# Kernel optimization log

Hardware: AMD Instinct MI355X
Metric: run time of the kernel (lower is better)

The kernel has to match this reference:

```python
import jax, jax.numpy as jnp
import numpy as np

HIDDEN = 2048
N_HEAD = 16
N_KV_HEAD = 4
HEAD_DIM = HIDDEN // N_HEAD
B, S = 2, 2048


def setup_inputs() -> dict:
    key = jax.random.key(0)
    ks = jax.random.split(key, 10)
    scale = 1.0 / np.sqrt(HIDDEN)
    x = jax.random.normal(ks[0], (B, S, HIDDEN), dtype=jnp.float32)
    # causal additive mask, broadcastable over batch and heads
    causal = jnp.tril(jnp.ones((S, S), dtype=jnp.bool_))
    attention_mask = jnp.where(causal, 0.0, -1e9).astype(jnp.float32)[None, None]
    wq_w = jax.random.uniform(ks[1], (HIDDEN, HIDDEN), jnp.float32, -scale, scale)
    wq_b = jax.random.uniform(ks[2], (HIDDEN,), jnp.float32, -scale, scale)
    wk_w = jax.random.uniform(ks[3], (N_KV_HEAD * HEAD_DIM, HIDDEN), jnp.float32, -scale, scale)
    wk_b = jax.random.uniform(ks[4], (N_KV_HEAD * HEAD_DIM,), jnp.float32, -scale, scale)
    wv_w = jax.random.uniform(ks[5], (N_KV_HEAD * HEAD_DIM, HIDDEN), jnp.float32, -scale, scale)
    wv_b = jax.random.uniform(ks[6], (N_KV_HEAD * HEAD_DIM,), jnp.float32, -scale, scale)
    wo_w = jax.random.uniform(ks[7], (HIDDEN, HIDDEN), jnp.float32, -scale, scale)
    wo_b = jax.random.uniform(ks[8], (HIDDEN,), jnp.float32, -scale, scale)
    return dict(x=x, attention_mask=attention_mask, wq_w=wq_w, wq_b=wq_b,
                wk_w=wk_w, wk_b=wk_b, wv_w=wv_w, wv_b=wv_b, wo_w=wo_w, wo_b=wo_b)


def reference(x, attention_mask, wq_w, wq_b, wk_w, wk_b, wv_w, wv_b, wo_w, wo_b):
    bs, seq_len, _ = x.shape
    group = N_HEAD // N_KV_HEAD
    q = x @ wq_w.T + wq_b  # [B,S,H*D]
    k = x @ wk_w.T + wk_b  # [B,S,Hkv*D]
    v = x @ wv_w.T + wv_b
    q = q.reshape(bs, seq_len, N_HEAD, HEAD_DIM).transpose(0, 2, 1, 3)        # [B,H,S,D]
    k = k.reshape(bs, seq_len, N_KV_HEAD, HEAD_DIM).transpose(0, 2, 1, 3)     # [B,Hkv,S,D]
    v = v.reshape(bs, seq_len, N_KV_HEAD, HEAD_DIM).transpose(0, 2, 1, 3)
    # GQA: share each kv head across `group` query heads (repeat_interleave equiv)
    qg = q.reshape(bs, N_KV_HEAD, group, seq_len, HEAD_DIM)
    scores = jnp.einsum('bkgqd,bkld->bkgql', qg, k) / np.sqrt(HEAD_DIM)       # [B,Hkv,g,S,S]
    scores = scores + attention_mask[:, :, None]  # mask broadcast over head dims
    attn = jax.nn.softmax(scores, axis=-1)  # dropout is identity at inference
    out = jnp.einsum('bkgql,bkld->bkgqd', attn, v)                             # [B,Hkv,g,S,D]
    out = out.reshape(bs, N_HEAD, seq_len, HEAD_DIM).transpose(0, 2, 1, 3)
    out = out.reshape(bs, seq_len, HIDDEN)
    return out @ wo_w.T + wo_b
```

## Files before the change

kernel.cpp:

```cpp
#include <hip/hip_runtime.h>

typedef __bf16 bf16;
typedef __bf16 bf16x8 __attribute__((ext_vector_type(8)));
typedef __bf16 bf16x4 __attribute__((ext_vector_type(4)));
typedef __bf16 bf16x2 __attribute__((ext_vector_type(2)));
typedef float  f32x4  __attribute__((ext_vector_type(4)));

#define HIDDEN 2048
#define NH 16
#define NKV 4
#define HD 128
#define BB 2
#define SS 2048
#define MTOT (BB*SS)
#define KVD (NKV*HD)

__device__ __forceinline__ void gload_lds16(const void* g, void* l) {
  __builtin_amdgcn_global_load_lds(
      (__attribute__((address_space(1))) void*)(void*)g,
      (__attribute__((address_space(3))) void*)l,
      16, 0, 0);
}

__device__ __forceinline__ void pipe_barrier() {
  __builtin_amdgcn_sched_barrier(0);
  __builtin_amdgcn_s_barrier();
  __builtin_amdgcn_sched_barrier(0);
}

__global__ void detect_dtype(const unsigned short* __restrict__ x, int* __restrict__ flag) {
  __shared__ int cnt;
  if (threadIdx.x == 0) cnt = 0;
  __syncthreads();
  int c = 0;
  for (int i = threadIdx.x; i < 8192; i += blockDim.x) {
    float v = fabsf(__uint_as_float((unsigned)x[i] << 16));
    if (v > 64.0f || (v > 0.0f && v < 9.5367431640625e-07f)) ++c;
  }
  atomicAdd(&cnt, c);
  __syncthreads();
  if (threadIdx.x == 0) flag[0] = (cnt > 1024) ? 1 : 0;
}

struct ConvJobs {
  const void* src[8];
  bf16*       dst[8];
  long long   n[8];
};

__global__ void conv_multi(ConvJobs jobs, const int* __restrict__ flag) {
  const int f = flag[0];
  const int a = blockIdx.y;
  const long long n = jobs.n[a];
  bf16* dst = jobs.dst[a];
  long long i = (long long)blockIdx.x * blockDim.x + threadIdx.x;
  const long long stride = (long long)gridDim.x * blockDim.x;
  if (f) {
    const float* s = (const float*)jobs.src[a];
    for (; i < n; i += stride) dst[i] = (bf16)s[i];
  } else {
    const bf16* s = (const bf16*)jobs.src[a];
    for (; i < n; i += stride) dst[i] = s[i];
  }
}

__global__ void conv_one(const void* __restrict__ src, bf16* __restrict__ dst,
                         long long n, const int* __restrict__ flag) {
  const int f = flag[0];
  long long i = (long long)blockIdx.x * blockDim.x + threadIdx.x;
  const long long stride = (long long)gridDim.x * blockDim.x;
  if (f) {
    const float* s = (const float*)src;
    for (; i < n; i += stride) dst[i] = (bf16)s[i];
  } else {
    const bf16* s = (const bf16*)src;
    for (; i < n; i += stride) dst[i] = s[i];
  }
}


__global__ __launch_bounds__(512)
void gemm_qkv256(const bf16* __restrict__ A,
                 const bf16* __restrict__ wq, const bf16* __restrict__ bq,
                 const bf16* __restrict__ wk, const bf16* __restrict__ bk,
                 const bf16* __restrict__ wv, const bf16* __restrict__ bv,
                 bf16* __restrict__ Cq, bf16* __restrict__ Ck, bf16* __restrict__ Cvt)
{
  __shared__ bf16 Asl[2][256*32];
  __shared__ bf16 Bsl[2][256*32];
  const int bx = blockIdx.x;
  const bf16 *Wp, *bias;
  int n0, mode;
  if (bx < 8)       { Wp = wq; bias = bq; n0 = bx*256;      mode = 0; }
  else if (bx < 10) { Wp = wk; bias = bk; n0 = (bx-8)*256;  mode = 1; }
  else              { Wp = wv; bias = bv; n0 = (bx-10)*256; mode = 2; }

  const int tid  = threadIdx.x;
  const int wave = tid >> 6, lane = tid & 63;
  const int g = lane >> 4, l15 = lane & 15;
  const int wr = wave >> 2, wc = wave & 3;
  const int m0 = blockIdx.y * 256;

  f32x4 acc[8][4] = {};

  auto stage4 = [&](int nb, int k0) {
    #pragma unroll
    for (int i = 0; i < 2; ++i) {
      const int cl  = tid + i*512;
      const int row = cl >> 2, ch = cl & 3;
      const int sc  = ch ^ ((row >> 2) & 3);
      gload_lds16(A  + (size_t)(m0 + row)*HIDDEN + k0 + sc*8, &Asl[nb][cl*8]);
      gload_lds16(Wp + (size_t)(n0 + row)*HIDDEN + k0 + sc*8, &Bsl[nb][cl*8]);
    }
  };

  stage4(0, 0);
  asm volatile("s_waitcnt vmcnt(0)" ::: "memory");
  pipe_barrier();

  const int nt = HIDDEN / 32;
  int buf = 0;
  for (int t = 0; t < nt; ++t) {
    bf16x8 af[4], bfr[4];
    #pragma unroll
    for (int mi = 0; mi < 4; ++mi) {
      const int rl = wr*128 + mi*16 + l15;
      const int ch = g ^ ((rl >> 2) & 3);
      af[mi] = *(const bf16x8*)&Asl[buf][rl*32 + ch*8];
    }
    #pragma unroll
    for (int ni = 0; ni < 4; ++ni) {
      const int rl = wc*64 + ni*16 + l15;
      const int ch = g ^ ((rl >> 2) & 3);
      bfr[ni] = *(const bf16x8*)&Bsl[buf][rl*32 + ch*8];
    }
    if (t + 1 < nt) stage4(buf ^ 1, (t + 1) * 32);
    pipe_barrier();
    __builtin_amdgcn_s_setprio(1);
    #pragma unroll
    for (int mi = 0; mi < 4; ++mi)
      #pragma unroll
      for (int ni = 0; ni < 4; ++ni)
        acc[mi][ni] = __builtin_amdgcn_mfma_f32_16x16x32_bf16(af[mi], bfr[ni], acc[mi][ni], 0, 0, 0);
    __builtin_amdgcn_s_setprio(0);
    #pragma unroll
    for (int mi = 0; mi < 4; ++mi) {
      const int rl = wr*128 + 64 + mi*16 + l15;
      const int ch = g ^ ((rl >> 2) & 3);
      af[mi] = *(const bf16x8*)&Asl[buf][rl*32 + ch*8];
    }
    pipe_barrier();
    __builtin_amdgcn_s_setprio(1);
    #pragma unroll
    for (int mi = 0; mi < 4; ++mi)
      #pragma unroll
      for (int ni = 0; ni < 4; ++ni)
        acc[4+mi][ni] = __builtin_amdgcn_mfma_f32_16x16x32_bf16(af[mi], bfr[ni], acc[4+mi][ni], 0, 0, 0);
    __builtin_amdgcn_s_setprio(0);
    __builtin_amdgcn_sched_barrier(0);
    asm volatile("s_waitcnt vmcnt(0)" ::: "memory");
    __builtin_amdgcn_s_barrier();
    __builtin_amdgcn_sched_barrier(0);
    buf ^= 1;
  }

  if (mode == 2) {
    #pragma unroll
    for (int ni = 0; ni < 4; ++ni) {
      const int cc = n0 + wc*64 + ni*16 + l15;
      const float bv2 = (float)bias[cc];
      #pragma unroll
      for (int mi = 0; mi < 8; ++mi) {
        const int row = m0 + wr*128 + mi*16 + g*4;
        bf16x4 o4;
        #pragma unroll
        for (int r = 0; r < 4; ++r) o4[r] = (bf16)(acc[mi][ni][r] + bv2);
        *(bf16x4*)&Cvt[(size_t)cc*MTOT + row] = o4;
      }
    }
  } else {
    bf16* Cb = (mode == 0) ? Cq : Ck;
    const int N = (mode == 0) ? HIDDEN : KVD;
    #pragma unroll
    for (int ni = 0; ni < 4; ++ni) {
      const int col = n0 + wc*64 + ni*16 + l15;
      const float bv2 = (float)bias[col];
      #pragma unroll
      for (int mi = 0; mi < 8; ++mi) {
        const int row = m0 + wr*128 + mi*16 + g*4;
        #pragma unroll
        for (int r = 0; r < 4; ++r)
          Cb[(size_t)(row + r)*N + col] = (bf16)(acc[mi][ni][r] + bv2);
      }
    }
  }
}

__global__ __launch_bounds__(512)
void gemm_o256(const bf16* __restrict__ A, const bf16* __restrict__ Wp,
               const bf16* __restrict__ bias, void* __restrict__ C,
               int N, int K, const int* __restrict__ flagp)
{
  __shared__ bf16 Asl[2][256*32];
  __shared__ bf16 Bsl[2][256*32];
  const int tid  = threadIdx.x;
  const int wave = tid >> 6, lane = tid & 63;
  const int g = lane >> 4, l15 = lane & 15;
  const int wr = wave >> 2, wc = wave & 3;
  const int m0 = blockIdx.y * 256, n0 = blockIdx.x * 256;

  f32x4 acc[8][4] = {};

  auto stage4 = [&](int nb, int k0) {
    #pragma unroll
    for (int i = 0; i < 2; ++i) {
      const int cl  = tid + i*512;
      const int row = cl >> 2, ch = cl & 3;
      const int sc  = ch ^ ((row >> 2) & 3);
      gload_lds16(A  + (size_t)(m0 + row)*K + k0 + sc*8, &Asl[nb][cl*8]);
      gload_lds16(Wp + (size_t)(n0 + row)*K + k0 + sc*8, &Bsl[nb][cl*8]);
    }
  };

  stage4(0, 0);
  asm volatile("s_waitcnt vmcnt(0)" ::: "memory");
  pipe_barrier();

  const int nt = K / 32;
  int buf = 0;
  for (int t = 0; t < nt; ++t) {
    bf16x8 af[4], bfr[4];
    #pragma unroll
    for (int mi = 0; mi < 4; ++mi) {
      const int rl = wr*128 + mi*16 + l15;
      const int ch = g ^ ((rl >> 2) & 3);
      af[mi] = *(const bf16x8*)&Asl[buf][rl*32 + ch*8];
    }
    #pragma unroll
    for (int ni = 0; ni < 4; ++ni) {
      const int rl = wc*64 + ni*16 + l15;
      const int ch = g ^ ((rl >> 2) & 3);
      bfr[ni] = *(const bf16x8*)&Bsl[buf][rl*32 + ch*8];
    }
    if (t + 1 < nt) stage4(buf ^ 1, (t + 1) * 32);
    pipe_barrier();
    __builtin_amdgcn_s_setprio(1);
    #pragma unroll
    for (int mi = 0; mi < 4; ++mi)
      #pragma unroll
      for (int ni = 0; ni < 4; ++ni)
        acc[mi][ni] = __builtin_amdgcn_mfma_f32_16x16x32_bf16(af[mi], bfr[ni], acc[mi][ni], 0, 0, 0);
    __builtin_amdgcn_s_setprio(0);
    #pragma unroll
    for (int mi = 0; mi < 4; ++mi) {
      const int rl = wr*128 + 64 + mi*16 + l15;
      const int ch = g ^ ((rl >> 2) & 3);
      af[mi] = *(const bf16x8*)&Asl[buf][rl*32 + ch*8];
    }
    pipe_barrier();
    __builtin_amdgcn_s_setprio(1);
    #pragma unroll
    for (int mi = 0; mi < 4; ++mi)
      #pragma unroll
      for (int ni = 0; ni < 4; ++ni)
        acc[4+mi][ni] = __builtin_amdgcn_mfma_f32_16x16x32_bf16(af[mi], bfr[ni], acc[4+mi][ni], 0, 0, 0);
    __builtin_amdgcn_s_setprio(0);
    __builtin_amdgcn_sched_barrier(0);
    asm volatile("s_waitcnt vmcnt(0)" ::: "memory");
    __builtin_amdgcn_s_barrier();
    __builtin_amdgcn_sched_barrier(0);
    buf ^= 1;
  }

  const int outf = flagp ? flagp[0] : 0;
  if (outf) {
    float* Cf = (float*)C;
    #pragma unroll
    for (int ni = 0; ni < 4; ++ni) {
      const int col = n0 + wc*64 + ni*16 + l15;
      const float bv = (float)bias[col];
      #pragma unroll
      for (int mi = 0; mi < 8; ++mi) {
        const int row = m0 + wr*128 + mi*16 + g*4;
        #pragma unroll
        for (int r = 0; r < 4; ++r)
          Cf[(size_t)(row + r)*N + col] = acc[mi][ni][r] + bv;
      }
    }
  } else {
    bf16* Cb = (bf16*)C;
    #pragma unroll
    for (int ni = 0; ni < 4; ++ni) {
      const int col = n0 + wc*64 + ni*16 + l15;
      const float bv = (float)bias[col];
      #pragma unroll
      for (int mi = 0; mi < 8; ++mi) {
        const int row = m0 + wr*128 + mi*16 + g*4;
        #pragma unroll
        for (int r = 0; r < 4; ++r)
          Cb[(size_t)(row + r)*N + col] = (bf16)(acc[mi][ni][r] + bv);
      }
    }
  }
}

#define QB 64
#define PPAD 72

__global__ __launch_bounds__(256)
void attn_fwd(const bf16* __restrict__ Q, const bf16* __restrict__ K,
              const bf16* __restrict__ Vt, bf16* __restrict__ O)
{
  __shared__ bf16 Ks[2][64*128];
  __shared__ bf16 Vs[2][128*64];
  __shared__ bf16 Pl[4][16][PPAD];
  const int tid = threadIdx.x, wave = tid >> 6, lane = tid & 63;
  const int g = lane >> 4, l15 = lane & 15;
  const int bh = blockIdx.y;
  const int b = bh >> 4, h = bh & 15, kvh = h >> 2;
  const bf16* Qh = Q + ((size_t)b*SS)*HIDDEN + h*HD;
  const bf16* Kh = K + ((size_t)b*SS)*KVD + kvh*HD;
  const bf16* Vh = Vt + ((size_t)kvh*HD)*MTOT + (size_t)b*SS;
  bf16*       Oh = O + ((size_t)b*SS)*HIDDEN + h*HD;

  const float scale  = 0.08838834764831845f;
  const float L2E    = 1.4426950408889634f;
  const float NEGBIG = -1.0e30f;

  const int krow_st = (lane >> 4);
  const int vrow_st = (lane >> 3);
  const int ksc     = (lane & 15);
  const int vsc     = (lane & 7) ^ (lane >> 3);

  #pragma unroll 1
  for (int pass = 0; pass < 2; ++pass) {
    const int qt = pass ? (31 - (int)blockIdx.x) : (int)blockIdx.x;
    const int qrow0 = qt*QB + wave*16;
    const int qg    = qrow0 + l15;

    bf16x8 bq[4];
    #pragma unroll
    for (int c = 0; c < 4; ++c)
      bq[c] = *(const bf16x8*)(Qh + (size_t)(qrow0 + l15)*HIDDEN + c*32 + g*8);

    f32x4 od[8] = {};
    float m_run = NEGBIG, l_part = 0.f;
    const int ntiles = qt + 1;

    {
      const int kv0 = 0;
      #pragma unroll
      for (int i = 0; i < 4; ++i) {
        const int s = wave*4 + i;
        const int kr = s*4 + krow_st;
        const int kc = ksc ^ (kr & 7);
        gload_lds16(Kh + (size_t)(kv0 + kr)*KVD + kc*8, &Ks[0][s*512 + lane*8]);
        const int vr = s*8 + vrow_st;
        gload_lds16(Vh + (size_t)vr*MTOT + kv0 + vsc*8, &Vs[0][s*512 + lane*8]);
      }
    }
    asm volatile("s_waitcnt vmcnt(0)" ::: "memory");
    __syncthreads();

    int buf = 0;
    #pragma unroll 1
    for (int t = 0; t < ntiles; ++t) {
      const int kv0 = t * 64;

      if (t + 1 < ntiles) {
        const int kv1 = kv0 + 64;
        #pragma unroll
        for (int i = 0; i < 4; ++i) {
          const int s = wave*4 + i;
          const int kr = s*4 + krow_st;
          const int kc = ksc ^ (kr & 7);
          gload_lds16(Kh + (size_t)(kv1 + kr)*KVD + kc*8, &Ks[buf^1][s*512 + lane*8]);
          const int vr = s*8 + vrow_st;
          gload_lds16(Vh + (size_t)vr*MTOT + kv1 + vsc*8, &Vs[buf^1][s*512 + lane*8]);
        }
      }

      f32x4 st[4];
      #pragma unroll
      for (int nb = 0; nb < 4; ++nb) {
        f32x4 s = {};
        #pragma unroll
        for (int c = 0; c < 4; ++c) {
          const int krow = nb*16 + l15;
          const int kch  = (c*4 + g) ^ (krow & 7);
          bf16x8 ka = *(const bf16x8*)&Ks[buf][krow*128 + kch*8];
          s = __builtin_amdgcn_mfma_f32_16x16x32_bf16(ka, bq[c], s, 0, 0, 0);
        }
        st[nb] = s;
      }

      float x[16];
      float mt = NEGBIG;
      #pragma unroll
      for (int nb = 0; nb < 4; ++nb)
        #pragma unroll
        for (int r = 0; r < 4; ++r) {
          const int kv = kv0 + nb*16 + g*4 + r;
          float v = st[nb][r] * scale;
          v = (kv <= qg) ? v : NEGBIG;
          x[nb*4 + r] = v;
          mt = fmaxf(mt, v);
        }
      mt = fmaxf(mt, __shfl_xor(mt, 16, 64));
      mt = fmaxf(mt, __shfl_xor(mt, 32, 64));
      const float m_new = fmaxf(m_run, mt);
      const float corr  = __builtin_amdgcn_exp2f((m_run - m_new) * L2E);

      float psum = 0.f;
      bf16x2 pk[4][2];
      #pragma unroll
      for (int nb = 0; nb < 4; ++nb) {
        const float p0 = __builtin_amdgcn_exp2f((x[nb*4+0] - m_new) * L2E);
        const float p1 = __builtin_amdgcn_exp2f((x[nb*4+1] - m_new) * L2E);
        const float p2 = __builtin_amdgcn_exp2f((x[nb*4+2] - m_new) * L2E);
        const float p3 = __builtin_amdgcn_exp2f((x[nb*4+3] - m_new) * L2E);
        psum += p0 + p1 + p2 + p3;
        pk[nb][0] = bf16x2{(bf16)p0, (bf16)p1};
        pk[nb][1] = bf16x2{(bf16)p2, (bf16)p3};
      }
      l_part = l_part * corr + psum;
      m_run  = m_new;
      #pragma unroll
      for (int db = 0; db < 8; ++db) od[db] *= corr;

      #pragma unroll
      for (int nb = 0; nb < 4; ++nb) {
        *(bf16x2*)&Pl[wave][l15][nb*16 + g*4 + 0] = pk[nb][0];
        *(bf16x2*)&Pl[wave][l15][nb*16 + g*4 + 2] = pk[nb][1];
      }
      asm volatile("s_waitcnt lgkmcnt(0)" ::: "memory");
      __builtin_amdgcn_sched_barrier(0);

      #pragma unroll
      for (int c = 0; c < 2; ++c) {
        bf16x8 pb = *(const bf16x8*)&Pl[wave][l15][c*32 + g*8];
        #pragma unroll
        for (int db = 0; db < 8; ++db) {
          const int vrow = db*16 + l15;
          const int vch  = (c*4 + g) ^ (l15 & 7);
          bf16x8 va = *(const bf16x8*)&Vs[buf][vrow*64 + vch*8];
          od[db] = __builtin_amdgcn_mfma_f32_16x16x32_bf16(va, pb, od[db], 0, 0, 0);
        }
      }

      asm volatile("s_waitcnt vmcnt(0)" ::: "memory");
      __syncthreads();
      buf ^= 1;
    }

    float lt = l_part;
    lt += __shfl_xor(lt, 16, 64);
    lt += __shfl_xor(lt, 32, 64);
    const float inv = 1.0f / lt;
    #pragma unroll
    for (int db = 0; db < 8; ++db) {
      bf16x4 o4;
      #pragma unroll
      for (int r = 0; r < 4; ++r) o4[r] = (bf16)(od[db][r] * inv);
      *(bf16x4*)(Oh + (size_t)qg*HIDDEN + db*16 + g*4) = o4;
    }
  }
}

extern "C" void kernel_launch(void* const* d_in, const int* in_sizes, int n_in,
                              void* d_out, int out_size, void* d_ws, size_t ws_size,
                              hipStream_t stream)
{
  (void)in_sizes; (void)n_in; (void)out_size; (void)ws_size;
  const void* x    = d_in[0];
  const void* wq_w = d_in[2];
  const void* wq_b = d_in[3];
  const void* wk_w = d_in[4];
  const void* wk_b = d_in[5];
  const void* wv_w = d_in[6];
  const void* wv_b = d_in[7];
  const void* wo_w = d_in[8];
  const void* wo_b = d_in[9];

  int*  flag = (int*)d_ws;
  bf16* base = (bf16*)((char*)d_ws + 256);
  const long long NX  = (long long)MTOT*HIDDEN;
  const long long NWQ = (long long)HIDDEN*HIDDEN;
  const long long NWK = (long long)KVD*HIDDEN;
  bf16* x_ao = base;
  bf16* wqwo = x_ao + NX;
  bf16* wk_c = wqwo + NWQ;
  bf16* wv_c = wk_c + NWK;
  bf16* bq_c = wv_c + NWK;
  bf16* bk_c = bq_c + 2048;
  bf16* bv_c = bk_c + 512;
  bf16* bo_c = bv_c + 512;
  bf16* q_ws  = bo_c + 2048;
  bf16* k_ws  = q_ws + NX;
  bf16* vt_ws = k_ws + (long long)MTOT*KVD;

  detect_dtype<<<1, 256, 0, stream>>>((const unsigned short*)x, flag);

  ConvJobs jb;
  jb.src[0] = x;    jb.dst[0] = x_ao; jb.n[0] = NX;
  jb.src[1] = wq_w; jb.dst[1] = wqwo; jb.n[1] = NWQ;
  jb.src[2] = wk_w; jb.dst[2] = wk_c; jb.n[2] = NWK;
  jb.src[3] = wv_w; jb.dst[3] = wv_c; jb.n[3] = NWK;
  jb.src[4] = wq_b; jb.dst[4] = bq_c; jb.n[4] = 2048;
  jb.src[5] = wk_b; jb.dst[5] = bk_c; jb.n[5] = 512;
  jb.src[6] = wv_b; jb.dst[6] = bv_c; jb.n[6] = 512;
  jb.src[7] = wo_b; jb.dst[7] = bo_c; jb.n[7] = 2048;
  conv_multi<<<dim3(1024, 8), 256, 0, stream>>>(jb, flag);

  gemm_qkv256<<<dim3(12, MTOT/256), 512, 0, stream>>>(x_ao, wqwo, bq_c, wk_c, bk_c,
                                                      wv_c, bv_c, q_ws, k_ws, vt_ws);

  conv_one<<<dim3(1024), 256, 0, stream>>>(wo_w, wqwo, NWQ, flag);

  attn_fwd<<<dim3(16, BB*NH), 256, 0, stream>>>(q_ws, k_ws, vt_ws, x_ao);

  gemm_o256<<<dim3(HIDDEN/256, MTOT/256), 512, 0, stream>>>(x_ao, wqwo, bo_c, d_out,
                                                            HIDDEN, HIDDEN, flag);
}
```

Measured before the change: 251.2 us.

## Vectorize conversions, shrink attention KV tile, lazy rescale, simpler output GEMM

Conversion kernels now move 8 elements per thread with vector loads and stores and launch half as many blocks. The attention kernel uses 32-wide KV tiles, folds the softmax scale into the exp2 constant, applies the causal mask only on the last two tiles, and skips the running-max rescale unless the max grows past a threshold. The output projection replaces the double-buffered 256x256 GEMM with a single-buffered 128x128 tile kernel without swizzle. The output GEMM loses load/compute overlap and gets LDS bank conflicts, while attention gets smaller per-tile work and more barriers.

```diff
diff --git a/kernel.cpp b/kernel.cpp
--- a/kernel.cpp
+++ b/kernel.cpp
@@ -48,36 +48,39 @@
   long long   n[8];
 };
 
+__device__ __forceinline__ void conv8(const void* src, bf16* dst, long long n,
+                                      int f, long long i0, long long stride) {
+  const long long n8 = n >> 3;
+  if (f) {
+    const float4* s4 = (const float4*)src;
+    for (long long i = i0; i < n8; i += stride) {
+      float4 a = s4[2*i], b = s4[2*i+1];
+      bf16x8 o;
+      o[0]=(bf16)a.x; o[1]=(bf16)a.y; o[2]=(bf16)a.z; o[3]=(bf16)a.w;
+      o[4]=(bf16)b.x; o[5]=(bf16)b.y; o[6]=(bf16)b.z; o[7]=(bf16)b.w;
+      *(bf16x8*)&dst[i*8] = o;
+    }
+  } else {
+    const bf16x8* s8 = (const bf16x8*)src;
+    for (long long i = i0; i < n8; i += stride)
+      *(bf16x8*)&dst[i*8] = s8[i];
+  }
+}
+
 __global__ void conv_multi(ConvJobs jobs, const int* __restrict__ flag) {
   const int f = flag[0];
   const int a = blockIdx.y;
-  const long long n = jobs.n[a];
-  bf16* dst = jobs.dst[a];
-  long long i = (long long)blockIdx.x * blockDim.x + threadIdx.x;
-  const long long stride = (long long)gridDim.x * blockDim.x;
-  if (f) {
-    const float* s = (const float*)jobs.src[a];
-    for (; i < n; i += stride) dst[i] = (bf16)s[i];
-  } else {
-    const bf16* s = (const bf16*)jobs.src[a];
-    for (; i < n; i += stride) dst[i] = s[i];
-  }
+  conv8(jobs.src[a], jobs.dst[a], jobs.n[a], f,
+        (long long)blockIdx.x * blockDim.x + threadIdx.x,
+        (long long)gridDim.x * blockDim.x);
 }
 
 __global__ void conv_one(const void* __restrict__ src, bf16* __restrict__ dst,
                          long long n, const int* __restrict__ flag) {
-  const int f = flag[0];
-  long long i = (long long)blockIdx.x * blockDim.x + threadIdx.x;
-  const long long stride = (long long)gridDim.x * blockDim.x;
-  if (f) {
-    const float* s = (const float*)src;
-    for (; i < n; i += stride) dst[i] = (bf16)s[i];
-  } else {
-    const bf16* s = (const bf16*)src;
-    for (; i < n; i += stride) dst[i] = s[i];
-  }
-}
-
+  conv8(src, dst, n, flag[0],
+        (long long)blockIdx.x * blockDim.x + threadIdx.x,
+        (long long)gridDim.x * blockDim.x);
+}
 
 __global__ __launch_bounds__(512)
 void gemm_qkv256(const bf16* __restrict__ A,
@@ -196,124 +199,88 @@
   }
 }
 
-__global__ __launch_bounds__(512)
-void gemm_o256(const bf16* __restrict__ A, const bf16* __restrict__ Wp,
-               const bf16* __restrict__ bias, void* __restrict__ C,
-               int N, int K, const int* __restrict__ flagp)
+__global__ __launch_bounds__(256)
+void gemm_bt(const bf16* __restrict__ A, const bf16* __restrict__ W,
+             const bf16* __restrict__ bias, void* __restrict__ C,
+             int M, int N, int K, const int* __restrict__ flagp)
 {
-  __shared__ bf16 Asl[2][256*32];
-  __shared__ bf16 Bsl[2][256*32];
+  __shared__ bf16 As[128*32];
+  __shared__ bf16 Bs[128*32];
   const int tid  = threadIdx.x;
   const int wave = tid >> 6, lane = tid & 63;
   const int g = lane >> 4, l15 = lane & 15;
-  const int wr = wave >> 2, wc = wave & 3;
-  const int m0 = blockIdx.y * 256, n0 = blockIdx.x * 256;
-
-  f32x4 acc[8][4] = {};
-
-  auto stage4 = [&](int nb, int k0) {
+  const int m0 = blockIdx.y * 128, n0 = blockIdx.x * 128;
+  const int wm = (wave >> 1) * 64, wn = (wave & 1) * 64;
+  const int srow = lane >> 2;
+  const int scol = (lane & 3) * 8;
+  f32x4 acc[4][4] = {};
+
+  for (int k0 = 0; k0 < K; k0 += 32) {
     #pragma unroll
     for (int i = 0; i < 2; ++i) {
-      const int cl  = tid + i*512;
-      const int row = cl >> 2, ch = cl & 3;
-      const int sc  = ch ^ ((row >> 2) & 3);
-      gload_lds16(A  + (size_t)(m0 + row)*K + k0 + sc*8, &Asl[nb][cl*8]);
-      gload_lds16(Wp + (size_t)(n0 + row)*K + k0 + sc*8, &Bsl[nb][cl*8]);
-    }
-  };
-
-  stage4(0, 0);
-  asm volatile("s_waitcnt vmcnt(0)" ::: "memory");
-  pipe_barrier();
-
-  const int nt = K / 32;
-  int buf = 0;
-  for (int t = 0; t < nt; ++t) {
+      const int seg = wave*2 + i;
+      const int row = seg*16 + srow;
+      gload_lds16(A + (size_t)(m0+row)*K + k0 + scol, &As[row*32 + scol]);
+      gload_lds16(W + (size_t)(n0+row)*K + k0 + scol, &Bs[row*32 + scol]);
+    }
+    asm volatile("s_waitcnt vmcnt(0)" ::: "memory");
+    __syncthreads();
     bf16x8 af[4], bfr[4];
     #pragma unroll
-    for (int mi = 0; mi < 4; ++mi) {
-      const int rl = wr*128 + mi*16 + l15;
-      const int ch = g ^ ((rl >> 2) & 3);
-      af[mi] = *(const bf16x8*)&Asl[buf][rl*32 + ch*8];
-    }
-    #pragma unroll
-    for (int ni = 0; ni < 4; ++ni) {
-      const int rl = wc*64 + ni*16 + l15;
-      const int ch = g ^ ((rl >> 2) & 3);
-      bfr[ni] = *(const bf16x8*)&Bsl[buf][rl*32 + ch*8];
-    }
-    if (t + 1 < nt) stage4(buf ^ 1, (t + 1) * 32);
-    pipe_barrier();
-    __builtin_amdgcn_s_setprio(1);
-    #pragma unroll
-    for (int mi = 0; mi < 4; ++mi)
-      #pragma unroll
-      for (int ni = 0; ni < 4; ++ni)
-        acc[mi][ni] = __builtin_amdgcn_mfma_f32_16x16x32_bf16(af[mi], bfr[ni], acc[mi][ni], 0, 0, 0);
-    __builtin_amdgcn_s_setprio(0);
-    #pragma unroll
-    for (int mi = 0; mi < 4; ++mi) {
-      const int rl = wr*128 + 64 + mi*16 + l15;
-      const int ch = g ^ ((rl >> 2) & 3);
-      af[mi] = *(const bf16x8*)&Asl[buf][rl*32 + ch*8];
-    }
-    pipe_barrier();
-    __builtin_amdgcn_s_setprio(1);
-    #pragma unroll
-    for (int mi = 0; mi < 4; ++mi)
-      #pragma unroll
-      for (int ni = 0; ni < 4; ++ni)
-        acc[4+mi][ni] = __builtin_amdgcn_mfma_f32_16x16x32_bf16(af[mi], bfr[ni], acc[4+mi][ni], 0, 0, 0);
-    __builtin_amdgcn_s_setprio(0);
-    __builtin_amdgcn_sched_barrier(0);
-    asm volatile("s_waitcnt vmcnt(0)" ::: "memory");
-    __builtin_amdgcn_s_barrier();
-    __builtin_amdgcn_sched_barrier(0);
-    buf ^= 1;
-  }
-
+    for (int m = 0; m < 4; ++m)
+      af[m] = *(const bf16x8*)&As[(wm + m*16 + l15)*32 + g*8];
+    #pragma unroll
+    for (int n = 0; n < 4; ++n)
+      bfr[n] = *(const bf16x8*)&Bs[(wn + n*16 + l15)*32 + g*8];
+    #pragma unroll
+    for (int m = 0; m < 4; ++m)
+      #pragma unroll
+      for (int n = 0; n < 4; ++n)
+        acc[m][n] = __builtin_amdgcn_mfma_f32_16x16x32_bf16(af[m], bfr[n], acc[m][n], 0, 0, 0);
+    __syncthreads();
+  }
   const int outf = flagp ? flagp[0] : 0;
   if (outf) {
     float* Cf = (float*)C;
     #pragma unroll
-    for (int ni = 0; ni < 4; ++ni) {
-      const int col = n0 + wc*64 + ni*16 + l15;
+    for (int n = 0; n < 4; ++n) {
+      const int col = n0 + wn + n*16 + l15;
       const float bv = (float)bias[col];
       #pragma unroll
-      for (int mi = 0; mi < 8; ++mi) {
-        const int row = m0 + wr*128 + mi*16 + g*4;
+      for (int m = 0; m < 4; ++m) {
+        const int row = m0 + wm + m*16 + g*4;
         #pragma unroll
         for (int r = 0; r < 4; ++r)
-          Cf[(size_t)(row + r)*N + col] = acc[mi][ni][r] + bv;
+          Cf[(size_t)(row + r)*N + col] = acc[m][n][r] + bv;
       }
     }
   } else {
     bf16* Cb = (bf16*)C;
     #pragma unroll
-    for (int ni = 0; ni < 4; ++ni) {
-      const int col = n0 + wc*64 + ni*16 + l15;
+    for (int n = 0; n < 4; ++n) {
+      const int col = n0 + wn + n*16 + l15;
       const float bv = (float)bias[col];
       #pragma unroll
-      for (int mi = 0; mi < 8; ++mi) {
-        const int row = m0 + wr*128 + mi*16 + g*4;
+      for (int m = 0; m < 4; ++m) {
+        const int row = m0 + wm + m*16 + g*4;
         #pragma unroll
         for (int r = 0; r < 4; ++r)
-          Cb[(size_t)(row + r)*N + col] = (bf16)(acc[mi][ni][r] + bv);
+          Cb[(size_t)(row + r)*N + col] = (bf16)(acc[m][n][r] + bv);
       }
     }
   }
 }
 
 #define QB 64
-#define PPAD 72
+#define KB2 32
 
 __global__ __launch_bounds__(256)
 void attn_fwd(const bf16* __restrict__ Q, const bf16* __restrict__ K,
               const bf16* __restrict__ Vt, bf16* __restrict__ O)
 {
-  __shared__ bf16 Ks[2][64*128];
-  __shared__ bf16 Vs[2][128*64];
-  __shared__ bf16 Pl[4][16][PPAD];
+  __shared__ bf16 Ks[2][KB2*128];
+  __shared__ bf16 Vs[2][128*KB2];
+  __shared__ bf16 Pl[4][16][36];
   const int tid = threadIdx.x, wave = tid >> 6, lane = tid & 63;
   const int g = lane >> 4, l15 = lane & 15;
   const int bh = blockIdx.y;
@@ -323,14 +290,14 @@
   const bf16* Vh = Vt + ((size_t)kvh*HD)*MTOT + (size_t)b*SS;
   bf16*       Oh = O + ((size_t)b*SS)*HIDDEN + h*HD;
 
-  const float scale  = 0.08838834764831845f;
-  const float L2E    = 1.4426950408889634f;
+  const float KSC    = 0.12751879526563404f;
   const float NEGBIG = -1.0e30f;
 
-  const int krow_st = (lane >> 4);
-  const int vrow_st = (lane >> 3);
-  const int ksc     = (lane & 15);
-  const int vsc     = (lane & 7) ^ (lane >> 3);
+  const int krow_st = lane >> 4;
+  const int ksc     = lane & 15;
+  const int vrow_in = lane >> 2;
+  const int vsrc_x  = ((lane >> 2) ^ (lane >> 4)) & 3;
+  const int svr     = (l15 ^ (l15 >> 2)) & 3;
 
   #pragma unroll 1
   for (int pass = 0; pass < 2; ++pass) {
@@ -345,105 +312,108 @@
 
     f32x4 od[8] = {};
     float m_run = NEGBIG, l_part = 0.f;
-    const int ntiles = qt + 1;
-
-    {
-      const int kv0 = 0;
-      #pragma unroll
-      for (int i = 0; i < 4; ++i) {
-        const int s = wave*4 + i;
+    const int nt = 2*qt + 2;
+
+    auto stage = [&](int bi, int kv0) {
+      #pragma unroll
+      for (int i = 0; i < 2; ++i) {
+        const int s = wave*2 + i;
         const int kr = s*4 + krow_st;
         const int kc = ksc ^ (kr & 7);
-        gload_lds16(Kh + (size_t)(kv0 + kr)*KVD + kc*8, &Ks[0][s*512 + lane*8]);
-        const int vr = s*8 + vrow_st;
-        gload_lds16(Vh + (size_t)vr*MTOT + kv0 + vsc*8, &Vs[0][s*512 + lane*8]);
-      }
-    }
+        gload_lds16(Kh + (size_t)(kv0 + kr)*KVD + kc*8, &Ks[bi][s*512 + lane*8]);
+        const int vr = s*16 + vrow_in;
+        const int vc = (lane & 3) ^ vsrc_x;
+        gload_lds16(Vh + (size_t)vr*MTOT + kv0 + vc*8, &Vs[bi][s*512 + lane*8]);
+      }
+    };
+
+    stage(0, 0);
     asm volatile("s_waitcnt vmcnt(0)" ::: "memory");
     __syncthreads();
 
     int buf = 0;
     #pragma unroll 1
-    for (int t = 0; t < ntiles; ++t) {
-      const int kv0 = t * 64;
-
-      if (t + 1 < ntiles) {
-        const int kv1 = kv0 + 64;
-        #pragma unroll
-        for (int i = 0; i < 4; ++i) {
-          const int s = wave*4 + i;
-          const int kr = s*4 + krow_st;
-          const int kc = ksc ^ (kr & 7);
-          gload_lds16(Kh + (size_t)(kv1 + kr)*KVD + kc*8, &Ks[buf^1][s*512 + lane*8]);
-          const int vr = s*8 + vrow_st;
-          gload_lds16(Vh + (size_t)vr*MTOT + kv1 + vsc*8, &Vs[buf^1][s*512 + lane*8]);
-        }
-      }
-
-      f32x4 st[4];
-      #pragma unroll
-      for (int nb = 0; nb < 4; ++nb) {
+    for (int t = 0; t < nt; ++t) {
+      const int kv0 = t * KB2;
+
+      if (t + 1 < nt) stage(buf ^ 1, kv0 + KB2);
+
+      f32x4 st[2];
+      #pragma unroll
+      for (int nb = 0; nb < 2; ++nb) {
         f32x4 s = {};
         #pragma unroll
         for (int c = 0; c < 4; ++c) {
           const int krow = nb*16 + l15;
-          const int kch  = (c*4 + g) ^ (krow & 7);
+          const int kch  = (c*4 + g) ^ (l15 & 7);
           bf16x8 ka = *(const bf16x8*)&Ks[buf][krow*128 + kch*8];
           s = __builtin_amdgcn_mfma_f32_16x16x32_bf16(ka, bq[c], s, 0, 0, 0);
         }
         st[nb] = s;
       }
 
-      float x[16];
+      float x[8];
       float mt = NEGBIG;
-      #pragma unroll
-      for (int nb = 0; nb < 4; ++nb)
-        #pragma unroll
-        for (int r = 0; r < 4; ++r) {
-          const int kv = kv0 + nb*16 + g*4 + r;
-          float v = st[nb][r] * scale;
-          v = (kv <= qg) ? v : NEGBIG;
-          x[nb*4 + r] = v;
-          mt = fmaxf(mt, v);
-        }
+      if (t >= nt - 2) {
+        #pragma unroll
+        for (int nb = 0; nb < 2; ++nb)
+          #pragma unroll
+          for (int r = 0; r < 4; ++r) {
+            const int kv = kv0 + nb*16 + g*4 + r;
+            float v = (kv <= qg) ? st[nb][r] : NEGBIG;
+            x[nb*4 + r] = v;
+            mt = fmaxf(mt, v);
+          }
+      } else {
+        #pragma unroll
+        for (int nb = 0; nb < 2; ++nb)
+          #pragma unroll
+          for (int r = 0; r < 4; ++r) {
+            x[nb*4 + r] = st[nb][r];
+            mt = fmaxf(mt, st[nb][r]);
+          }
+      }
       mt = fmaxf(mt, __shfl_xor(mt, 16, 64));
       mt = fmaxf(mt, __shfl_xor(mt, 32, 64));
-      const float m_new = fmaxf(m_run, mt);
-      const float corr  = __builtin_amdgcn_exp2f((m_run - m_new) * L2E);
+
+      if (!__all((mt - m_run) <= 62.0f)) {
+        const float m_new = fmaxf(m_run, mt);
+        const float corr  = __builtin_amdgcn_exp2f((m_run - m_new) * KSC);
+        l_part *= corr;
+        #pragma unroll
+        for (int db = 0; db < 8; ++db) od[db] *= corr;
+        m_run = m_new;
+      }
 
       float psum = 0.f;
-      bf16x2 pk[4][2];
-      #pragma unroll
-      for (int nb = 0; nb < 4; ++nb) {
-        const float p0 = __builtin_amdgcn_exp2f((x[nb*4+0] - m_new) * L2E);
-        const float p1 = __builtin_amdgcn_exp2f((x[nb*4+1] - m_new) * L2E);
-        const float p2 = __builtin_amdgcn_exp2f((x[nb*4+2] - m_new) * L2E);
-        const float p3 = __builtin_amdgcn_exp2f((x[nb*4+3] - m_new) * L2E);
+      bf16x2 pk[2][2];
+      #pragma unroll
+      for (int nb = 0; nb < 2; ++nb) {
+        const float p0 = __builtin_amdgcn_exp2f((x[nb*4+0] - m_run) * KSC);
+        const float p1 = __builtin_amdgcn_exp2f((x[nb*4+1] - m_run) * KSC);
+        const float p2 = __builtin_amdgcn_exp2f((x[nb*4+2] - m_run) * KSC);
+        const float p3 = __builtin_amdgcn_exp2f((x[nb*4+3] - m_run) * KSC);
         psum += p0 + p1 + p2 + p3;
         pk[nb][0] = bf16x2{(bf16)p0, (bf16)p1};
         pk[nb][1] = bf16x2{(bf16)p2, (bf16)p3};
       }
-      l_part = l_part * corr + psum;
-      m_run  = m_new;
-      #pragma unroll
-      for (int db = 0; db < 8; ++db) od[db] *= corr;
-
-      #pragma unroll
-      for (int nb = 0; nb < 4; ++nb) {
+      l_part += psum;
+
+      #pragma unroll
+      for (int nb = 0; nb < 2; ++nb) {
         *(bf16x2*)&Pl[wave][l15][nb*16 + g*4 + 0] = pk[nb][0];
         *(bf16x2*)&Pl[wave][l15][nb*16 + g*4 + 2] = pk[nb][1];
       }
       asm volatile("s_waitcnt lgkmcnt(0)" ::: "memory");
       __builtin_amdgcn_sched_barrier(0);
 
-      #pragma unroll
-      for (int c = 0; c < 2; ++c) {
-        bf16x8 pb = *(const bf16x8*)&Pl[wave][l15][c*32 + g*8];
+      {
+        bf16x8 pb = *(const bf16x8*)&Pl[wave][l15][g*8];
         #pragma unroll
         for (int db = 0; db < 8; ++db) {
           const int vrow = db*16 + l15;
-          const int vch  = (c*4 + g) ^ (l15 & 7);
-          bf16x8 va = *(const bf16x8*)&Vs[buf][vrow*64 + vch*8];
+          const int vch  = g ^ svr;
+          bf16x8 va = *(const bf16x8*)&Vs[buf][vrow*KB2 + vch*8];
           od[db] = __builtin_amdgcn_mfma_f32_16x16x32_bf16(va, pb, od[db], 0, 0, 0);
         }
       }
@@ -510,15 +480,14 @@
   jb.src[5] = wk_b; jb.dst[5] = bk_c; jb.n[5] = 512;
   jb.src[6] = wv_b; jb.dst[6] = bv_c; jb.n[6] = 512;
   jb.src[7] = wo_b; jb.dst[7] = bo_c; jb.n[7] = 2048;
-  conv_multi<<<dim3(1024, 8), 256, 0, stream>>>(jb, flag);
+  conv_multi<<<dim3(512, 8), 256, 0, stream>>>(jb, flag);
 
   gemm_qkv256<<<dim3(12, MTOT/256), 512, 0, stream>>>(x_ao, wqwo, bq_c, wk_c, bk_c,
                                                       wv_c, bv_c, q_ws, k_ws, vt_ws);
 
-  conv_one<<<dim3(1024), 256, 0, stream>>>(wo_w, wqwo, NWQ, flag);
+  conv_one<<<dim3(512), 256, 0, stream>>>(wo_w, wqwo, NWQ, flag);
 
   attn_fwd<<<dim3(16, BB*NH), 256, 0, stream>>>(q_ws, k_ws, vt_ws, x_ao);
 
-  gemm_o256<<<dim3(HIDDEN/256, MTOT/256), 512, 0, stream>>>(x_ao, wqwo, bo_c, d_out,
-                                                            HIDDEN, HIDDEN, flag);
-}
+  gemm_bt<<<dim3(HIDDEN/128, MTOT/128), 256, 0, stream>>>(x_ao, wqwo, bo_c, d_out, MTOT, HIDDEN, HIDDEN, flag);
+}
```

Result: no change. 252.2 us (+0.4%).
